# Optimization experiments

Hardware: AMD Instinct MI355X
Metric: run time of the kernel (lower is better)

The kernel has to match this reference:

```python
import jax, jax.numpy as jnp
import numpy as np

INPUT_SIZE = (224, 224)


def setup_inputs() -> dict:
    key = jax.random.key(0)
    k1, k2, k3 = jax.random.split(key, 3)
    feat2 = jax.random.normal(k1, (16, 512, 28, 28), dtype=jnp.float32)
    feat3 = jax.random.normal(k2, (16, 1024, 14, 14), dtype=jnp.float32)
    memory_bank = jax.random.normal(k3, (16384, 1536), dtype=jnp.float32)
    return {"feat2": feat2, "feat3": feat3, "memory_bank": memory_bank}


def reference(feat2, feat3, memory_bank):
    b, c2, h, w = feat2.shape
    c3 = feat3.shape[1]
    # interpolate(feat3, size=(h,w), mode='bilinear', align_corners=False)
    feat3_up = jax.image.resize(feat3, (b, c3, h, w), method='bilinear')
    features = jnp.concatenate([feat2, feat3_up], axis=1)  # [b, c, h, w]
    c = c2 + c3
    feats = features.transpose(0, 2, 3, 1).reshape(-1, c)  # [N, c]
    x_sq = jnp.sum(feats * feats, axis=1, keepdims=True)            # [N, 1]
    m_sq = jnp.sum(memory_bank * memory_bank, axis=1)[None, :]      # [1, M]
    d2 = x_sq + m_sq - 2.0 * (feats @ memory_bank.T)                # [N, M]
    min_d = jnp.sqrt(jnp.maximum(jnp.min(d2, axis=1), 0.0))         # [N]
    anomaly_map = min_d.reshape(b, 1, h, w)
    anomaly_map = jax.image.resize(
        anomaly_map, (b, 1, INPUT_SIZE[0], INPUT_SIZE[1]), method='bilinear')
    pred_score = jnp.max(anomaly_map.reshape(b, -1), axis=1)
    return anomaly_map, pred_score
```

## Files before the change

kernel.cpp:

```cpp
#include <hip/hip_runtime.h>
#include <math.h>

#define N_ROWS 12544
#define C_DIM  1536
#define M_ROWS 16384
#define BATCH  16

#define QS    16.0f
#define S2x2  0.0078125f
#define S2    0.00390625f

typedef int   i32x4 __attribute__((ext_vector_type(4)));
typedef unsigned char u8;
typedef signed char   i8;

__device__ __forceinline__ unsigned fkey(float f) {
  unsigned u = __float_as_uint(f);
  return (u & 0x80000000u) ? ~u : (u | 0x80000000u);
}
__device__ __forceinline__ float funkey(unsigned k) {
  unsigned u = (k & 0x80000000u) ? (k ^ 0x80000000u) : ~k;
  return __uint_as_float(u);
}

__device__ __forceinline__ void gl_lds16(const void* g, void* l) {
  __builtin_amdgcn_global_load_lds(
      (__attribute__((address_space(1))) void*)(g),
      (__attribute__((address_space(3))) void*)(l), 16, 0, 0);
}

__device__ __forceinline__ int quant(float v) {
  int q = __float2int_rn(v * QS);
  return max(-127, min(127, q));
}

#define FSTRIDE 528

__global__ __launch_bounds__(512) void prep_all(
    const float* __restrict__ feat2, const float* __restrict__ feat3,
    const float* __restrict__ mb,
    i8* __restrict__ feats, i8* __restrict__ mbb,
    int* __restrict__ xsqi, float* __restrict__ msq) {
  const int blk = blockIdx.x;
  const int t = threadIdx.x;
  __shared__ u8 fsm[28 * FSTRIDE];
  __shared__ int sxq[28];

  if (blk >= 1344) {
    const int wave = t >> 6, lane = t & 63;
    const int row = (blk - 1344) * 8 + wave;
    const float* in = mb + (size_t)row * C_DIM;
    i8* outp = mbb + (size_t)row * C_DIM;
    float ssq = 0.f;
#pragma unroll
    for (int i = 0; i < 6; i++) {
      const int f4 = lane + 64 * i;
      const float4 v = *(const float4*)(in + f4 * 4);
      int q0 = quant(v.x), q1 = quant(v.y), q2 = quant(v.z), q3 = quant(v.w);
      unsigned w = (unsigned)(q0 & 0xFF) | ((unsigned)(q1 & 0xFF) << 8)
                 | ((unsigned)(q2 & 0xFF) << 16) | ((unsigned)(q3 & 0xFF) << 24);
      *(unsigned*)(outp + f4 * 4) = w;
      ssq += (float)(q0*q0 + q1*q1 + q2*q2 + q3*q3);
    }
    for (int off = 32; off > 0; off >>= 1) ssq += __shfl_down(ssq, off, 64);
    if (lane == 0) msq[row] = S2 * ssq;
  } else {
    const int half = blk % 3, p = blk / 3;
    const int b = p / 28, y = p % 28;
    const int n0 = b * 784 + y * 28;

    const float sy = 0.5f * y - 0.25f;
    const int y0 = (int)floorf(sy); const float fy = sy - (float)y0;
    const int y0c = max(y0, 0), y1c = min(y0 + 1, 13);
    const float wy0 = 1.f - fy, wy1 = fy;

    const int g  = t >> 5;
    const int l2 = t & 31;
    const float sx = 0.5f * l2 - 0.25f;
    const int x0 = (int)floorf(sx); const float fx = sx - (float)x0;
    const int x0c = max(x0, 0), x1c = min(x0 + 1, 13);
    const float wx0 = 1.f - fx, wx1 = fx;

    if (t < 28) sxq[t] = 0;

    if (half == 0) {
      const float* f2b = feat2 + (size_t)b * 512 * 784 + y * 28;
#pragma unroll 4
      for (int i = 0; i < 32; i++) {
        const int c = i * 16 + g;
        if (l2 < 28) {
          float v = f2b[(size_t)c * 784 + l2];
          fsm[l2 * FSTRIDE + c] = (u8)(i8)quant(v);
        }
      }
    } else {
      const int cc0 = (half - 1) * 512;
      const float* f3b = feat3 + (size_t)b * 1024 * 196;
#pragma unroll 4
      for (int i = 0; i < 32; i++) {
        const int cc = cc0 + i * 16 + g;
        const float* f3 = f3b + (size_t)cc * 196;
        float v = 0.f;
        if (l2 < 14)       v = f3[y0c * 14 + l2];
        else if (l2 < 28)  v = f3[y1c * 14 + (l2 - 14)];
        float t0 = wy0 * __shfl(v, x0c, 32)     + wy1 * __shfl(v, 14 + x0c, 32);
        float t1 = wy0 * __shfl(v, x1c, 32)     + wy1 * __shfl(v, 14 + x1c, 32);
        if (l2 < 28) {
          float o = wx0 * t0 + wx1 * t1;
          fsm[l2 * FSTRIDE + (i * 16 + g)] = (u8)(i8)quant(o);
        }
      }
    }
    __syncthreads();

    const int c0 = half * 512;
    i8* orow = feats + (size_t)n0 * C_DIM + c0;
    for (int idx = t; idx < 28 * 32; idx += 512) {
      const int row = idx / 32, col = idx % 32;
      i32x4 wv = *(const i32x4*)(fsm + row * FSTRIDE + col * 16);
      *(i32x4*)(orow + (size_t)row * C_DIM + col * 16) = wv;
      int s = 0;
#pragma unroll
      for (int k = 0; k < 4; k++) {
        const int w = wv[k];
        const int b0 = (int)(i8)(w & 0xFF), b1 = (int)(i8)((w >> 8) & 0xFF);
        const int b2 = (int)(i8)((w >> 16) & 0xFF), b3 = (int)(i8)(w >> 24);
        s += b0*b0 + b1*b1 + b2*b2 + b3*b3;
      }
      atomicAdd(&sxq[row], s);
    }
    __syncthreads();
    if (t < 28) atomicAdd(&xsqi[n0 + t], sxq[t]);
  }
}

__global__ void gemm_min(const i8* __restrict__ X, const i8* __restrict__ Mb,
                         const float* __restrict__ msq,
                         unsigned* __restrict__ dmin) {
  __shared__ u8 As[16384];
  __shared__ u8 Bs[16384];
  __shared__ unsigned smin[128];
  const int t = threadIdx.x;
  const int bx = blockIdx.x;
  const int mtile = ((bx & 7) << 4) | (bx >> 3);
  const int ntile = blockIdx.y;
  const int lane = t & 63, wave = t >> 6;
  const int wm = wave >> 1, wn = wave & 1;
  if (t < 128) smin[t] = 0xFFFFFFFFu;

  const int row0 = ntile * 128;
  const int col0 = mtile * 128;
  const int s_row = t >> 2;
  const int s_ch  = (t & 3) ^ ((t >> 3) & 3);
  const i8* ga = X  + (size_t)(row0 + s_row) * C_DIM + s_ch * 16;
  const i8* gb = Mb + (size_t)(col0 + s_row) * C_DIM + s_ch * 16;
  u8* la = As + t * 16;
  u8* lb = Bs + t * 16;

  i32x4 acc[4][4];
  const i32x4 zero = {0, 0, 0, 0};
#pragma unroll
  for (int mi = 0; mi < 4; mi++)
#pragma unroll
    for (int ni = 0; ni < 4; ni++) acc[mi][ni] = zero;

  const int quad = lane >> 4, l16 = lane & 15;
  const int fsw = (l16 >> 1) & 3;
  const int slot = ((quad ^ fsw) * 16);
  const u8* arow = As + (wm * 64 + l16) * 64 + slot;
  const u8* brow = Bs + (wn * 64 + l16) * 64 + slot;

  for (int k0 = 0; k0 < C_DIM; k0 += 128) {
    __syncthreads();
    gl_lds16(ga + k0,                    la);
    gl_lds16(ga + 64 * C_DIM + k0,       la + 4096);
    gl_lds16(ga + k0 + 64,               la + 8192);
    gl_lds16(ga + 64 * C_DIM + k0 + 64,  la + 12288);
    gl_lds16(gb + k0,                    lb);
    gl_lds16(gb + 64 * C_DIM + k0,       lb + 4096);
    gl_lds16(gb + k0 + 64,               lb + 8192);
    gl_lds16(gb + 64 * C_DIM + k0 + 64,  lb + 12288);
    __syncthreads();
#pragma unroll
    for (int sub = 0; sub < 2; sub++) {
      i32x4 af[4], bf[4];
#pragma unroll
      for (int mi = 0; mi < 4; mi++)
        af[mi] = *(const i32x4*)(arow + sub * 8192 + mi * 1024);
#pragma unroll
      for (int ni = 0; ni < 4; ni++)
        bf[ni] = *(const i32x4*)(brow + sub * 8192 + ni * 1024);
#pragma unroll
      for (int mi = 0; mi < 4; mi++)
#pragma unroll
        for (int ni = 0; ni < 4; ni++)
          acc[mi][ni] = __builtin_amdgcn_mfma_i32_16x16x64_i8(
              af[mi], bf[ni], acc[mi][ni], 0, 0, 0);
    }
  }

  float msql[4];
#pragma unroll
  for (int ni = 0; ni < 4; ni++)
    msql[ni] = msq[col0 + wn * 64 + ni * 16 + l16];

#pragma unroll
  for (int mi = 0; mi < 4; mi++) {
#pragma unroll
    for (int r = 0; r < 4; r++) {
      float v = msql[0] - S2x2 * (float)acc[mi][0][r];
#pragma unroll
      for (int ni = 1; ni < 4; ni++)
        v = fminf(v, msql[ni] - S2x2 * (float)acc[mi][ni][r]);
      v = fminf(v, __shfl_xor(v, 1, 64));
      v = fminf(v, __shfl_xor(v, 2, 64));
      v = fminf(v, __shfl_xor(v, 4, 64));
      v = fminf(v, __shfl_xor(v, 8, 64));
      if (l16 == 0) {
        int lrow = wm * 64 + mi * 16 + quad * 4 + r;
        atomicMin(&smin[lrow], fkey(v));
      }
    }
  }
  __syncthreads();
  if (t < 128) atomicMin(&dmin[row0 + t], smin[t]);
}

__global__ void finalize(const unsigned* __restrict__ dmin,
                         const int* __restrict__ xsqi,
                         float* __restrict__ out) {
  const int b = blockIdx.x, slice = blockIdx.y, t = threadIdx.x;
  __shared__ float smap[784];
  __shared__ float sred[4];
  for (int i = t; i < 784; i += 256) {
    float d2 = S2 * (float)xsqi[b * 784 + i] + funkey(dmin[b * 784 + i]);
    smap[i] = sqrtf(fmaxf(d2, 0.f));
  }
  __syncthreads();
  float* omap = out + (size_t)b * 50176;
  float tmax = 0.f;
  const int p0 = slice * 6272;
  for (int p = p0 + t; p < p0 + 6272; p += 256) {
    const int Y = p / 224, Xp = p % 224;
    const float sy = Y * 0.125f - 0.4375f;
    const float sx = Xp * 0.125f - 0.4375f;
    const int y0 = (int)floorf(sy); const float fy = sy - (float)y0;
    const int x0 = (int)floorf(sx); const float fx = sx - (float)x0;
    const int y0c = max(y0, 0), y1c = min(y0 + 1, 27);
    const int x0c = max(x0, 0), x1c = min(x0 + 1, 27);
    float v = (1.f-fy)*((1.f-fx)*smap[y0c*28+x0c] + fx*smap[y0c*28+x1c])
            +      fy *((1.f-fx)*smap[y1c*28+x0c] + fx*smap[y1c*28+x1c]);
    omap[p] = v;
    tmax = fmaxf(tmax, v);
  }
  for (int off = 32; off > 0; off >>= 1)
    tmax = fmaxf(tmax, __shfl_down(tmax, off, 64));
  if ((t & 63) == 0) sred[t >> 6] = tmax;
  __syncthreads();
  if (t == 0) {
    float m = fmaxf(fmaxf(sred[0], sred[1]), fmaxf(sred[2], sred[3]));
    atomicMax((unsigned*)(out + 802816 + b), __float_as_uint(m));
  }
}

extern "C" void kernel_launch(void* const* d_in, const int* in_sizes, int n_in,
                              void* d_out, int out_size, void* d_ws, size_t ws_size,
                              hipStream_t stream) {
  const float* feat2 = (const float*)d_in[0];
  const float* feat3 = (const float*)d_in[1];
  const float* mb    = (const float*)d_in[2];
  char* ws = (char*)d_ws;
  i8*       feats = (i8*)ws;
  i8*       mbb   = (i8*)(ws + 19267584);
  int*      xsqi  = (int*)(ws + 44433408);
  float*    msq   = (float*)(ws + 44483584);
  unsigned* dmin  = (unsigned*)(ws + 44549120);
  float* out = (float*)d_out;

  hipMemsetAsync(xsqi, 0, N_ROWS * 4, stream);
  hipMemsetAsync(dmin, 0xFF, N_ROWS * 4, stream);
  hipMemsetAsync(out + 802816, 0, BATCH * 4, stream);
  prep_all<<<1344 + 2048, 512, 0, stream>>>(
      feat2, feat3, mb, feats, mbb, xsqi, msq);
  gemm_min<<<dim3(128, 98), 256, 0, stream>>>(feats, mbb, msq, dmin);
  finalize<<<dim3(BATCH, 8), 256, 0, stream>>>(dmin, xsqi, out);
}
```

Baseline: 512.8 us.

## Load GEMM B fragments straight to registers and fold memsets into prep kernel

The memory-bank B fragments in the int8 GEMM are now read from global memory directly into registers, bypassing LDS. This halves LDS use per block and adds a launch bound requesting three blocks per CU to raise occupancy. The three hipMemsetAsync calls are removed. Their work moves into prep_all, which writes per-half partial row norms (summed later in finalize) and initialises dmin and the score slots. The risk is that uncoalesced per-lane global loads for B and more register pressure may offset the LDS and occupancy gains.

```diff
diff --git a/kernel.cpp b/kernel.cpp
--- a/kernel.cpp
+++ b/kernel.cpp
@@ -40,7 +40,8 @@
     const float* __restrict__ feat2, const float* __restrict__ feat3,
     const float* __restrict__ mb,
     i8* __restrict__ feats, i8* __restrict__ mbb,
-    int* __restrict__ xsqi, float* __restrict__ msq) {
+    int* __restrict__ xsqp, float* __restrict__ msq,
+    unsigned* __restrict__ dmin, unsigned* __restrict__ score) {
   const int blk = blockIdx.x;
   const int t = threadIdx.x;
   __shared__ u8 fsm[28 * FSTRIDE];
@@ -130,15 +131,18 @@
       atomicAdd(&sxq[row], s);
     }
     __syncthreads();
-    if (t < 28) atomicAdd(&xsqi[n0 + t], sxq[t]);
-  }
-}
-
-__global__ void gemm_min(const i8* __restrict__ X, const i8* __restrict__ Mb,
-                         const float* __restrict__ msq,
-                         unsigned* __restrict__ dmin) {
+    if (t < 28) {
+      xsqp[half * N_ROWS + n0 + t] = sxq[t];
+      if (half == 0) dmin[n0 + t] = 0xFFFFFFFFu;
+    }
+    if (blk == 0 && t < BATCH) score[t] = 0u;
+  }
+}
+
+__global__ __launch_bounds__(256, 3) void gemm_min(
+    const i8* __restrict__ X, const i8* __restrict__ Mb,
+    const float* __restrict__ msq, unsigned* __restrict__ dmin) {
   __shared__ u8 As[16384];
-  __shared__ u8 Bs[16384];
   __shared__ unsigned smin[128];
   const int t = threadIdx.x;
   const int bx = blockIdx.x;
@@ -152,10 +156,11 @@
   const int col0 = mtile * 128;
   const int s_row = t >> 2;
   const int s_ch  = (t & 3) ^ ((t >> 3) & 3);
-  const i8* ga = X  + (size_t)(row0 + s_row) * C_DIM + s_ch * 16;
-  const i8* gb = Mb + (size_t)(col0 + s_row) * C_DIM + s_ch * 16;
+  const i8* ga = X + (size_t)(row0 + s_row) * C_DIM + s_ch * 16;
   u8* la = As + t * 16;
-  u8* lb = Bs + t * 16;
+
+  const int quad = lane >> 4, l16 = lane & 15;
+  const i8* gbf = Mb + (size_t)(col0 + wn * 64 + l16) * C_DIM + quad * 16;
 
   i32x4 acc[4][4];
   const i32x4 zero = {0, 0, 0, 0};
@@ -164,11 +169,9 @@
 #pragma unroll
     for (int ni = 0; ni < 4; ni++) acc[mi][ni] = zero;
 
-  const int quad = lane >> 4, l16 = lane & 15;
   const int fsw = (l16 >> 1) & 3;
   const int slot = ((quad ^ fsw) * 16);
   const u8* arow = As + (wm * 64 + l16) * 64 + slot;
-  const u8* brow = Bs + (wn * 64 + l16) * 64 + slot;
 
   for (int k0 = 0; k0 < C_DIM; k0 += 128) {
     __syncthreads();
@@ -176,26 +179,25 @@
     gl_lds16(ga + 64 * C_DIM + k0,       la + 4096);
     gl_lds16(ga + k0 + 64,               la + 8192);
     gl_lds16(ga + 64 * C_DIM + k0 + 64,  la + 12288);
-    gl_lds16(gb + k0,                    lb);
-    gl_lds16(gb + 64 * C_DIM + k0,       lb + 4096);
-    gl_lds16(gb + k0 + 64,               lb + 8192);
-    gl_lds16(gb + 64 * C_DIM + k0 + 64,  lb + 12288);
+    i32x4 bf[2][4];
+#pragma unroll
+    for (int sub = 0; sub < 2; sub++)
+#pragma unroll
+      for (int ni = 0; ni < 4; ni++)
+        bf[sub][ni] = *(const i32x4*)(gbf + ni * (16 * C_DIM) + k0 + sub * 64);
     __syncthreads();
 #pragma unroll
     for (int sub = 0; sub < 2; sub++) {
-      i32x4 af[4], bf[4];
+      i32x4 af[4];
 #pragma unroll
       for (int mi = 0; mi < 4; mi++)
         af[mi] = *(const i32x4*)(arow + sub * 8192 + mi * 1024);
 #pragma unroll
-      for (int ni = 0; ni < 4; ni++)
-        bf[ni] = *(const i32x4*)(brow + sub * 8192 + ni * 1024);
-#pragma unroll
       for (int mi = 0; mi < 4; mi++)
 #pragma unroll
         for (int ni = 0; ni < 4; ni++)
           acc[mi][ni] = __builtin_amdgcn_mfma_i32_16x16x64_i8(
-              af[mi], bf[ni], acc[mi][ni], 0, 0, 0);
+              af[mi], bf[sub][ni], acc[mi][ni], 0, 0, 0);
     }
   }
 
@@ -227,13 +229,15 @@
 }
 
 __global__ void finalize(const unsigned* __restrict__ dmin,
-                         const int* __restrict__ xsqi,
+                         const int* __restrict__ xsqp,
                          float* __restrict__ out) {
   const int b = blockIdx.x, slice = blockIdx.y, t = threadIdx.x;
   __shared__ float smap[784];
   __shared__ float sred[4];
   for (int i = t; i < 784; i += 256) {
-    float d2 = S2 * (float)xsqi[b * 784 + i] + funkey(dmin[b * 784 + i]);
+    const int idx = b * 784 + i;
+    const int xs = xsqp[idx] + xsqp[N_ROWS + idx] + xsqp[2 * N_ROWS + idx];
+    float d2 = S2 * (float)xs + funkey(dmin[idx]);
     smap[i] = sqrtf(fmaxf(d2, 0.f));
   }
   __syncthreads();
@@ -272,16 +276,14 @@
   char* ws = (char*)d_ws;
   i8*       feats = (i8*)ws;
   i8*       mbb   = (i8*)(ws + 19267584);
-  int*      xsqi  = (int*)(ws + 44433408);
-  float*    msq   = (float*)(ws + 44483584);
-  unsigned* dmin  = (unsigned*)(ws + 44549120);
+  int*      xsqp  = (int*)(ws + 44433408);
+  float*    msq   = (float*)(ws + 44583936);
+  unsigned* dmin  = (unsigned*)(ws + 44649472);
   float* out = (float*)d_out;
 
-  hipMemsetAsync(xsqi, 0, N_ROWS * 4, stream);
-  hipMemsetAsync(dmin, 0xFF, N_ROWS * 4, stream);
-  hipMemsetAsync(out + 802816, 0, BATCH * 4, stream);
   prep_all<<<1344 + 2048, 512, 0, stream>>>(
-      feat2, feat3, mb, feats, mbb, xsqi, msq);
+      feat2, feat3, mb, feats, mbb, xsqp, msq, dmin,
+      (unsigned*)(out + 802816));
   gemm_min<<<dim3(128, 98), 256, 0, stream>>>(feats, mbb, msq, dmin);
-  finalize<<<dim3(BATCH, 8), 256, 0, stream>>>(dmin, xsqi, out);
-}
+  finalize<<<dim3(BATCH, 8), 256, 0, stream>>>(dmin, xsqp, out);
+}
```

Result: slower. 794.9 us (+55.0%).
